# Optimization experiments

Hardware: AMD Instinct MI355X
Metric: run time of the kernel (lower is better)

The kernel has to match this reference:

```python
import jax, jax.numpy as jnp
import numpy as np

D = 512      # d_model
H = 8        # num_heads
DH = D // H  # d_head = 64
WIN = 10     # window_size
DFF = 2048   # d_ff
EPS = 1e-5   # LayerNorm eps


def _layernorm(x, w, b):
    mu = jnp.mean(x, axis=-1, keepdims=True)
    var = jnp.mean(jnp.square(x - mu), axis=-1, keepdims=True)
    return (x - mu) * jax.lax.rsqrt(var + EPS) * w + b


def setup_inputs() -> dict:
    key = jax.random.key(0)
    ks = jax.random.split(key, 8)
    s = 0.02
    inp = {
        "z": jax.random.normal(ks[0], (4, 2048, D), jnp.float32),
        "Wq": jax.random.normal(ks[1], (D, D), jnp.float32) * s,
        "bq": jnp.zeros((D,), jnp.float32),
        "Wk": jax.random.normal(ks[2], (D, D), jnp.float32) * s,
        "bk": jnp.zeros((D,), jnp.float32),
        "Wv": jax.random.normal(ks[3], (D, D), jnp.float32) * s,
        "bv": jnp.zeros((D,), jnp.float32),
        "Wo": jax.random.normal(ks[4], (D, D), jnp.float32) * s,
        "bo": jnp.zeros((D,), jnp.float32),
        "ln1_w": jnp.ones((D,), jnp.float32),
        "ln1_b": jnp.zeros((D,), jnp.float32),
        "W1": jax.random.normal(ks[5], (D, DFF), jnp.float32) * s,
        "b1": jnp.zeros((DFF,), jnp.float32),
        "W2": jax.random.normal(ks[6], (DFF, D), jnp.float32) * s,
        "b2": jnp.zeros((D,), jnp.float32),
        "ln2_w": jnp.ones((D,), jnp.float32),
        "ln2_b": jnp.zeros((D,), jnp.float32),
    }
    return inp


def reference(z, Wq, bq, Wk, bk, Wv, bv, Wo, bo, ln1_w, ln1_b, W1, b1, W2, b2, ln2_w, ln2_b):
    B, T, Dm = z.shape
    # projections -> [B, H, T, DH]
    q = (z @ Wq + bq).reshape(B, T, H, DH).transpose(0, 2, 1, 3)
    k = (z @ Wk + bk).reshape(B, T, H, DH).transpose(0, 2, 1, 3)
    v = (z @ Wv + bv).reshape(B, T, H, DH).transpose(0, 2, 1, 3)
    scale = 1.0 / jnp.sqrt(jnp.asarray(DH, z.dtype))
    scores = jnp.einsum('bhqd,bhkd->bhqk', q, k) * scale  # [B,H,T,T]
    idx = jnp.arange(T)
    dist = idx[:, None] - idx[None, :]
    valid = (dist >= 0) & (dist < WIN)
    neg = jnp.finfo(scores.dtype).min
    scores = jnp.where(valid[None, None], scores, neg)
    attn = jax.nn.softmax(scores, axis=-1)  # dropout is identity in eval
    out = jnp.einsum('bhqk,bhkd->bhqd', attn, v)
    out = out.transpose(0, 2, 1, 3).reshape(B, T, Dm)
    out = out @ Wo + bo
    z = _layernorm(z + out, ln1_w, ln1_b)
    # FFN with exact (erf) GELU, matching torch nn.GELU default
    ff = jax.nn.gelu(z @ W1 + b1, approximate=False) @ W2 + b2
    z = _layernorm(z + ff, ln2_w, ln2_b)
    return z
```

## Files before the change

### kernel.cpp

```cpp
#include <hip/hip_runtime.h>
#include <cstdint>
#include <cstddef>

#define DEV __device__ __forceinline__

typedef __bf16 bf16x8 __attribute__((ext_vector_type(8)));
typedef float f32x4 __attribute__((ext_vector_type(4)));
typedef unsigned short us8 __attribute__((ext_vector_type(8)));
typedef unsigned short us4 __attribute__((ext_vector_type(4)));

typedef const __attribute__((address_space(1))) unsigned int GUI;
typedef __attribute__((address_space(3))) unsigned int LUI;

DEV unsigned short f2bf(float f) {
  unsigned int u = __builtin_bit_cast(unsigned int, f);
  u += 0x7fffu + ((u >> 16) & 1u);
  return (unsigned short)(u >> 16);
}
DEV float bf2f(unsigned short h) {
  unsigned int u = ((unsigned int)h) << 16;
  return __builtin_bit_cast(float, u);
}

DEV void tr32(const float* __restrict__ in, unsigned short* __restrict__ out,
              int K, int N, int k0, int n0) {
  __shared__ float tile[32][33];
  const int tx = threadIdx.x & 31, ty = threadIdx.x >> 5;
#pragma unroll
  for (int i = 0; i < 32; i += 8)
    tile[ty + i][tx] = in[(size_t)(k0 + ty + i) * N + n0 + tx];
  __syncthreads();
#pragma unroll
  for (int i = 0; i < 32; i += 8)
    out[(size_t)(n0 + ty + i) * K + k0 + tx] = f2bf(tile[tx][ty + i]);
}

__global__ __launch_bounds__(256) void k_prep(
    const float* __restrict__ z, unsigned short* __restrict__ zb,
    const float* __restrict__ Wq, const float* __restrict__ Wk,
    const float* __restrict__ Wv, const float* __restrict__ Wo,
    unsigned short* __restrict__ Wsq,
    const float* __restrict__ W1, unsigned short* __restrict__ W1T,
    const float* __restrict__ W2, unsigned short* __restrict__ W2T,
    const float* __restrict__ bq, const float* __restrict__ bk,
    const float* __restrict__ bv, float* __restrict__ biasqkv) {
  const int j = blockIdx.x;
  const int tid = threadIdx.x;
  if (j < 4096) {
    int i = j * 256 + tid;
    float4 v = ((const float4*)z)[i];
    us4 o;
    o.x = f2bf(v.x); o.y = f2bf(v.y); o.z = f2bf(v.z); o.w = f2bf(v.w);
    *(us4*)(zb + (size_t)i * 4) = o;
  } else if (j < 5120) {
    int t = j - 4096;
    int mat = t >> 8, tile = t & 255;
    const float* in = mat == 0 ? Wq : mat == 1 ? Wk : mat == 2 ? Wv : Wo;
    tr32(in, Wsq + (size_t)mat * 262144, 512, 512, (tile >> 4) * 32, (tile & 15) * 32);
  } else if (j < 6144) {
    int t = j - 5120;
    tr32(W1, W1T, 512, 2048, (t / 64) * 32, (t % 64) * 32);
  } else if (j < 7168) {
    int t = j - 6144;
    tr32(W2, W2T, 2048, 512, (t / 16) * 32, (t % 16) * 32);
  } else {
    for (int i = tid; i < 1536; i += 256)
      biasqkv[i] = (i < 512) ? bq[i] : (i < 1024 ? bk[i - 512] : bv[i - 1024]);
  }
}

template <int MODE, int SPLITK>
DEV void gemm_body(const unsigned short* __restrict__ A,
                   const unsigned short* __restrict__ BT,
                   const float* __restrict__ bias,
                   unsigned short* __restrict__ outp,
                   int K, int N) {
  __shared__ __align__(16) unsigned short As[2 * 16384];
  __shared__ __align__(16) unsigned short Bs[2 * 16384];
  const int tid = threadIdx.x;
  const int wave = tid >> 6, lane = tid & 63;
  const int wm = wave >> 2, wn = wave & 3;
  const int q = lane >> 4, l15 = lane & 15;

  const int nx = gridDim.x, ny = gridDim.y;
  const int nwg = nx * ny * SPLITK;
  const int lid = (blockIdx.z * ny + blockIdx.y) * nx + blockIdx.x;
  const int q8 = nwg >> 3, r8 = nwg & 7;
  const int xcd = lid & 7, slot = lid >> 3;
  const int wid = (xcd < r8 ? xcd * (q8 + 1) : r8 * (q8 + 1) + (xcd - r8) * q8) + slot;
  const int nbz = nx * SPLITK;
  const int bxz = wid % nbz;
  const int by  = wid / nbz;
  const int bx  = bxz % nx;
  const int z   = bxz / nx;

  const int rbase = by * 256;
  const int nbase = bx * 256;
  const int nkt = (K / SPLITK) >> 6;
  const int kb = z * (K / SPLITK);

  float bv_[4];
#pragma unroll
  for (int n = 0; n < 4; ++n) {
    int gcol = nbase + wn * 64 + n * 16 + l15;
    bv_[n] = (z == 0) ? bias[gcol] : 0.f;
  }
  asm volatile("s_waitcnt vmcnt(0)" ::: "memory");

  auto STAGE2 = [&](int buf, int k0, int t0) {
#pragma unroll
    for (int t = t0; t < t0 + 2; ++t) {
      int s = t * 512 + tid;
      int row = s >> 3;
      int col = ((s & 7) ^ (row & 7)) << 3;
      const unsigned short* ga = A + (size_t)(rbase + row) * K + k0 + col;
      const unsigned short* gb = BT + (size_t)(nbase + row) * K + k0 + col;
      const int dst = buf * 16384 + (t * 512 + wave * 64) * 8;
      __builtin_amdgcn_global_load_lds((GUI*)ga, (LUI*)(As + dst), 16, 0, 0);
      __builtin_amdgcn_global_load_lds((GUI*)gb, (LUI*)(Bs + dst), 16, 0, 0);
    }
  };

  auto LDA = [&](const unsigned short* Ab, int ks, int mh, bf16x8* af) {
#pragma unroll
    for (int m = 0; m < 4; ++m) {
      int row = wm * 128 + (mh * 4 + m) * 16 + l15;
      int ch = (ks * 4 + q) ^ (row & 7);
      af[m] = __builtin_bit_cast(bf16x8, *(const us8*)(Ab + row * 64 + ch * 8));
    }
  };
  auto LDB = [&](const unsigned short* Bb, int ks, bf16x8* bfr) {
#pragma unroll
    for (int n = 0; n < 4; ++n) {
      int row = wn * 64 + n * 16 + l15;
      int ch = (ks * 4 + q) ^ (row & 7);
      bfr[n] = __builtin_bit_cast(bf16x8, *(const us8*)(Bb + row * 64 + ch * 8));
    }
  };

  f32x4 acc[8][4] = {};
  bf16x8 af[4], bfr0[4], bfr1[4];

  STAGE2(0, kb, 0);
  STAGE2(0, kb, 2);
  asm volatile("s_waitcnt vmcnt(0)" ::: "memory");
  __builtin_amdgcn_s_barrier();

#define PHASE_TAIL                                     \
  asm volatile("s_waitcnt lgkmcnt(0)" ::: "memory");   \
  __builtin_amdgcn_sched_barrier(0);                   \
  __builtin_amdgcn_s_setprio(1);

#define MFMA16(AF, BF, MH)                                                        \
  _Pragma("unroll") for (int m = 0; m < 4; ++m)                                   \
  _Pragma("unroll") for (int n = 0; n < 4; ++n)                                   \
    acc[MH * 4 + m][n] = __builtin_amdgcn_mfma_f32_16x16x32_bf16(AF[m], BF[n], acc[MH * 4 + m][n], 0, 0, 0);

  for (int t = 0; t < nkt; ++t) {
    const int cur = t & 1;
    const unsigned short* Ab = As + cur * 16384;
    const unsigned short* Bb = Bs + cur * 16384;
    const bool pre = (t + 1 < nkt);
    const int knext = kb + (t + 1) * 64;

    LDA(Ab, 0, 0, af);
    LDB(Bb, 0, bfr0);
    if (pre) STAGE2(cur ^ 1, knext, 0);
    __builtin_amdgcn_s_barrier();
    PHASE_TAIL
    MFMA16(af, bfr0, 0)
    __builtin_amdgcn_s_setprio(0);
    __builtin_amdgcn_s_barrier();

    LDA(Ab, 1, 0, af);
    LDB(Bb, 1, bfr1);
    if (pre) STAGE2(cur ^ 1, knext, 2);
    __builtin_amdgcn_s_barrier();
    PHASE_TAIL
    MFMA16(af, bfr1, 0)
    __builtin_amdgcn_s_setprio(0);
    __builtin_amdgcn_s_barrier();

    LDA(Ab, 0, 1, af);
    __builtin_amdgcn_s_barrier();
    PHASE_TAIL
    MFMA16(af, bfr0, 1)
    __builtin_amdgcn_s_setprio(0);
    __builtin_amdgcn_s_barrier();

    LDA(Ab, 1, 1, af);
    if (pre) asm volatile("s_waitcnt vmcnt(0)" ::: "memory");
    __builtin_amdgcn_s_barrier();
    PHASE_TAIL
    MFMA16(af, bfr1, 1)
    __builtin_amdgcn_s_setprio(0);
    __builtin_amdgcn_s_barrier();
  }
#undef PHASE_TAIL
#undef MFMA16

  unsigned short* opv = outp + (size_t)z * 8192 * N;
#pragma unroll
  for (int m = 0; m < 8; ++m) {
    int grow0 = rbase + wm * 128 + m * 16 + (q << 2);
#pragma unroll
    for (int n = 0; n < 4; ++n) {
      int gcol = nbase + wn * 64 + n * 16 + l15;
#pragma unroll
      for (int r = 0; r < 4; ++r) {
        float v = acc[m][n][r] + bv_[n];
        if (MODE == 2) v = 0.5f * v * (1.0f + erff(v * 0.70710678118654752f));
        opv[(size_t)(grow0 + r) * N + gcol] = f2bf(v);
      }
    }
  }
}

__global__ __launch_bounds__(512) void k_qkv(const unsigned short* __restrict__ A,
                                             const unsigned short* __restrict__ BT,
                                             const float* __restrict__ bias,
                                             unsigned short* __restrict__ outp, int K, int N) {
  gemm_body<0, 1>(A, BT, bias, outp, K, N);
}
__global__ __launch_bounds__(512) void k_wo(const unsigned short* __restrict__ A,
                                            const unsigned short* __restrict__ BT,
                                            const float* __restrict__ bias,
                                            unsigned short* __restrict__ outp, int K, int N) {
  gemm_body<0, 4>(A, BT, bias, outp, K, N);
}
__global__ __launch_bounds__(512) void k_ffn1(const unsigned short* __restrict__ A,
                                              const unsigned short* __restrict__ BT,
                                              const float* __restrict__ bias,
                                              unsigned short* __restrict__ outp, int K, int N) {
  gemm_body<2, 1>(A, BT, bias, outp, K, N);
}
__global__ __launch_bounds__(512) void k_ffn2(const unsigned short* __restrict__ A,
                                              const unsigned short* __restrict__ BT,
                                              const float* __restrict__ bias,
                                              unsigned short* __restrict__ outp, int K, int N) {
  gemm_body<0, 4>(A, BT, bias, outp, K, N);
}

__global__ __launch_bounds__(64) void k_attn(const unsigned short* __restrict__ qkv,
                                             unsigned short* __restrict__ attnb) {
  __shared__ float Qt[64 * 35];
  __shared__ float Kt[64 * 45];
  __shared__ float P[32 * 12];

  const int lane = threadIdx.x;
  const int bid = blockIdx.x;
  const int chunk = bid & 63;
  const int bh = bid >> 6;
  const int h = bh & 7, b = bh >> 3;
  const int i0 = chunk * 32;
  const int b2048 = b * 2048;
  const int h64 = h * 64;

#pragma unroll 8
  for (int r = 0; r < 41; ++r) {
    int jloc = i0 - 9 + r;
    int jc = jloc < 0 ? 0 : jloc;
    Kt[lane * 45 + r] = bf2f(qkv[(size_t)(b2048 + jc) * 1536 + 512 + h64 + lane]);
  }
#pragma unroll 8
  for (int r = 0; r < 32; ++r) {
    Qt[lane * 35 + r] = bf2f(qkv[(size_t)(b2048 + i0 + r) * 1536 + h64 + lane]);
  }
  __syncthreads();

  const int qe = lane & 31, dh = lane >> 5;
  float s[10];
#pragma unroll
  for (int jj = 0; jj < 10; ++jj) s[jj] = 0.f;
#pragma unroll
  for (int dd = 0; dd < 32; ++dd) {
    int d = dh * 32 + dd;
    float qd = Qt[d * 35 + qe];
#pragma unroll
    for (int jj = 0; jj < 10; ++jj)
      s[jj] = fmaf(qd, Kt[d * 45 + qe + jj], s[jj]);
  }
#pragma unroll
  for (int jj = 0; jj < 10; ++jj) s[jj] += __shfl_xor(s[jj], 32);

  const int iG = i0 + qe;
#pragma unroll
  for (int jj = 0; jj < 10; ++jj)
    s[jj] = (iG - 9 + jj >= 0) ? s[jj] * 0.125f : -1e30f;
  float mx = s[9];
#pragma unroll
  for (int jj = 0; jj < 9; ++jj) mx = fmaxf(mx, s[jj]);
  float den = 0.f;
#pragma unroll
  for (int jj = 0; jj < 10; ++jj) {
    s[jj] = __expf(s[jj] - mx);
    den += s[jj];
  }
  float inv = 1.f / den;
  if (lane < 32) {
#pragma unroll
    for (int jj = 0; jj < 10; ++jj) P[qe * 12 + jj] = s[jj] * inv;
  }
  __syncthreads();

  for (int q0 = 0; q0 < 32; q0 += 4) {
    float vv[13];
#pragma unroll
    for (int t = 0; t < 13; ++t) {
      int jloc = i0 + q0 - 9 + t;
      int jc = jloc < 0 ? 0 : jloc;
      vv[t] = bf2f(qkv[(size_t)(b2048 + jc) * 1536 + 1024 + h64 + lane]);
    }
#pragma unroll
    for (int qq = 0; qq < 4; ++qq) {
      const int qy = q0 + qq;
      const float* pp = &P[qy * 12];
      float o = 0.f;
#pragma unroll
      for (int jj = 0; jj < 10; ++jj) o = fmaf(pp[jj], vv[qq + jj], o);
      attnb[(size_t)(b2048 + i0 + qy) * 512 + h64 + lane] = f2bf(o);
    }
  }
}

template <int OUTF32, int NP>
DEV void ln_body(const unsigned short* __restrict__ res,
                 const unsigned short* __restrict__ add,
                 const float* __restrict__ w,
                 const float* __restrict__ bb,
                 void* __restrict__ outp) {
  const size_t PLANE = (size_t)8192 * 512;
  const int wave = threadIdx.x >> 6, lane = threadIdx.x & 63;
  const int row = blockIdx.x * 4 + wave;
  float x[8];
  us8 r = *(const us8*)(res + (size_t)row * 512 + lane * 8);
#pragma unroll
  for (int j = 0; j < 8; ++j) x[j] = bf2f(r[j]);
#pragma unroll
  for (int p = 0; p < NP; ++p) {
    us8 a = *(const us8*)(add + p * PLANE + (size_t)row * 512 + lane * 8);
#pragma unroll
    for (int j = 0; j < 8; ++j) x[j] += bf2f(a[j]);
  }
  float sum = 0.f, ss = 0.f;
#pragma unroll
  for (int j = 0; j < 8; ++j) {
    sum += x[j];
    ss += x[j] * x[j];
  }
#pragma unroll
  for (int m = 32; m >= 1; m >>= 1) {
    sum += __shfl_xor(sum, m);
    ss += __shfl_xor(ss, m);
  }
  const float mu = sum * (1.f / 512.f);
  float var = ss * (1.f / 512.f) - mu * mu;
  const float rstd = rsqrtf(var + 1e-5f);
  const int c = lane * 8;
  float o[8];
#pragma unroll
  for (int j = 0; j < 8; ++j) o[j] = (x[j] - mu) * rstd * w[c + j] + bb[c + j];
  if (OUTF32 == 0) {
    us8 u;
#pragma unroll
    for (int j = 0; j < 8; ++j) u[j] = f2bf(o[j]);
    *(us8*)((unsigned short*)outp + (size_t)row * 512 + c) = u;
  } else {
    float4 u0, u1;
    u0.x = o[0]; u0.y = o[1]; u0.z = o[2]; u0.w = o[3];
    u1.x = o[4]; u1.y = o[5]; u1.z = o[6]; u1.w = o[7];
    float4* o4 = (float4*)((float*)outp + (size_t)row * 512 + c);
    o4[0] = u0; o4[1] = u1;
  }
}

__global__ __launch_bounds__(256) void k_ln_mid(const unsigned short* __restrict__ res,
                                                const unsigned short* __restrict__ add,
                                                const float* __restrict__ w,
                                                const float* __restrict__ bb,
                                                unsigned short* __restrict__ outp) {
  ln_body<0, 4>(res, add, w, bb, outp);
}
__global__ __launch_bounds__(256) void k_ln_out(const unsigned short* __restrict__ res,
                                                const unsigned short* __restrict__ add,
                                                const float* __restrict__ w,
                                                const float* __restrict__ bb,
                                                float* __restrict__ outp) {
  ln_body<1, 4>(res, add, w, bb, outp);
}

extern "C" void kernel_launch(void* const* d_in, const int* in_sizes, int n_in,
                              void* d_out, int out_size, void* d_ws, size_t ws_size,
                              hipStream_t stream) {
  const float* z    = (const float*)d_in[0];
  const float* Wq   = (const float*)d_in[1];
  const float* bq   = (const float*)d_in[2];
  const float* Wk   = (const float*)d_in[3];
  const float* bk   = (const float*)d_in[4];
  const float* Wv   = (const float*)d_in[5];
  const float* bv   = (const float*)d_in[6];
  const float* Wo   = (const float*)d_in[7];
  const float* bo   = (const float*)d_in[8];
  const float* ln1w = (const float*)d_in[9];
  const float* ln1b = (const float*)d_in[10];
  const float* W1   = (const float*)d_in[11];
  const float* b1   = (const float*)d_in[12];
  const float* W2   = (const float*)d_in[13];
  const float* b2   = (const float*)d_in[14];
  const float* ln2w = (const float*)d_in[15];
  const float* ln2b = (const float*)d_in[16];
  float* out = (float*)d_out;

  char* ws = (char*)d_ws;
  size_t off = 0;
  auto alloc = [&](size_t bytes) {
    char* p = ws + off;
    off += (bytes + 255) & ~(size_t)255;
    return p;
  };
  unsigned short* Wsq   = (unsigned short*)alloc((size_t)2048 * 512 * 2);
  unsigned short* WTqkv = Wsq;
  unsigned short* WoT   = Wsq + (size_t)1536 * 512;
  unsigned short* W1T   = (unsigned short*)alloc((size_t)2048 * 512 * 2);
  unsigned short* W2T   = (unsigned short*)alloc((size_t)512 * 2048 * 2);
  float*          biasqkv = (float*)alloc(1536 * 4);
  unsigned short* zb    = (unsigned short*)alloc((size_t)8192 * 512 * 2);
  unsigned short* z1b   = (unsigned short*)alloc((size_t)8192 * 512 * 2);
  unsigned short* qkvb  = (unsigned short*)alloc((size_t)8192 * 1536 * 2);
  unsigned short* attnb = (unsigned short*)alloc((size_t)8192 * 512 * 2);
  unsigned short* p1    = (unsigned short*)alloc((size_t)4 * 8192 * 512 * 2);
  unsigned short* ff    = qkvb;

  k_prep<<<7169, 256, 0, stream>>>(z, zb, Wq, Wk, Wv, Wo, Wsq, W1, W1T, W2, W2T,
                                   bq, bk, bv, biasqkv);
  k_qkv<<<dim3(6, 32), 512, 0, stream>>>(zb, WTqkv, biasqkv, qkvb, 512, 1536);
  k_attn<<<2048, 64, 0, stream>>>(qkvb, attnb);
  k_wo<<<dim3(2, 32, 4), 512, 0, stream>>>(attnb, WoT, bo, p1, 512, 512);
  k_ln_mid<<<2048, 256, 0, stream>>>(zb, p1, ln1w, ln1b, z1b);
  k_ffn1<<<dim3(8, 32), 512, 0, stream>>>(z1b, W1T, b1, ff, 512, 2048);
  k_ffn2<<<dim3(2, 32, 4), 512, 0, stream>>>(ff, W2T, b2, p1, 2048, 512);
  k_ln_out<<<2048, 256, 0, stream>>>(z1b, p1, ln2w, ln2b, out);
}
```

Before: 145.0 us.

## Switch GEMM to four-stage K=32 LDS pipeline with precomputed addresses

Restructures the GEMM main loop from a double-buffered K=64 tile to a four-slot ring buffer of K=32 tiles, prefetching three tiles ahead and waiting with partial vmcnt counts instead of full drains. It changes the LDS layout so two rows share a 64-element line, and precomputes the global and LDS fragment offsets once outside the loop. The goal is to hide global-load latency better and cut per-iteration address arithmetic. In exchange there are twice as many iterations with barriers, and the hand-tuned vmcnt counts must exactly match the number of loads still in flight.

Measured after the change: 147.1 us. Within noise of the previous version (+1.4%).

```diff
diff --git a/kernel.cpp b/kernel.cpp
--- a/kernel.cpp
+++ b/kernel.cpp
@@ -75,8 +75,8 @@
                    const float* __restrict__ bias,
                    unsigned short* __restrict__ outp,
                    int K, int N) {
-  __shared__ __align__(16) unsigned short As[2 * 16384];
-  __shared__ __align__(16) unsigned short Bs[2 * 16384];
+  __shared__ __align__(16) unsigned short As[4 * 8192];
+  __shared__ __align__(16) unsigned short Bs[4 * 8192];
   const int tid = threadIdx.x;
   const int wave = tid >> 6, lane = tid & 63;
   const int wm = wave >> 2, wn = wave & 3;
@@ -86,8 +86,8 @@
   const int nwg = nx * ny * SPLITK;
   const int lid = (blockIdx.z * ny + blockIdx.y) * nx + blockIdx.x;
   const int q8 = nwg >> 3, r8 = nwg & 7;
-  const int xcd = lid & 7, slot = lid >> 3;
-  const int wid = (xcd < r8 ? xcd * (q8 + 1) : r8 * (q8 + 1) + (xcd - r8) * q8) + slot;
+  const int xcd = lid & 7, slot0 = lid >> 3;
+  const int wid = (xcd < r8 ? xcd * (q8 + 1) : r8 * (q8 + 1) + (xcd - r8) * q8) + slot0;
   const int nbz = nx * SPLITK;
   const int bxz = wid % nbz;
   const int by  = wid / nbz;
@@ -96,7 +96,7 @@
 
   const int rbase = by * 256;
   const int nbase = bx * 256;
-  const int nkt = (K / SPLITK) >> 6;
+  const int nkt = (K / SPLITK) >> 5;
   const int kb = z * (K / SPLITK);
 
   float bv_[4];
@@ -107,97 +107,107 @@
   }
   asm volatile("s_waitcnt vmcnt(0)" ::: "memory");
 
-  auto STAGE2 = [&](int buf, int k0, int t0) {
-#pragma unroll
-    for (int t = t0; t < t0 + 2; ++t) {
-      int s = t * 512 + tid;
-      int row = s >> 3;
-      int col = ((s & 7) ^ (row & 7)) << 3;
-      const unsigned short* ga = A + (size_t)(rbase + row) * K + k0 + col;
-      const unsigned short* gb = BT + (size_t)(nbase + row) * K + k0 + col;
-      const int dst = buf * 16384 + (t * 512 + wave * 64) * 8;
-      __builtin_amdgcn_global_load_lds((GUI*)ga, (LUI*)(As + dst), 16, 0, 0);
-      __builtin_amdgcn_global_load_lds((GUI*)gb, (LUI*)(Bs + dst), 16, 0, 0);
-    }
-  };
-
-  auto LDA = [&](const unsigned short* Ab, int ks, int mh, bf16x8* af) {
-#pragma unroll
-    for (int m = 0; m < 4; ++m) {
-      int row = wm * 128 + (mh * 4 + m) * 16 + l15;
-      int ch = (ks * 4 + q) ^ (row & 7);
-      af[m] = __builtin_bit_cast(bf16x8, *(const us8*)(Ab + row * 64 + ch * 8));
-    }
-  };
-  auto LDB = [&](const unsigned short* Bb, int ks, bf16x8* bfr) {
-#pragma unroll
-    for (int n = 0; n < 4; ++n) {
-      int row = wn * 64 + n * 16 + l15;
-      int ch = (ks * 4 + q) ^ (row & 7);
-      bfr[n] = __builtin_bit_cast(bf16x8, *(const us8*)(Bb + row * 64 + ch * 8));
-    }
-  };
+  const unsigned short* pA[2];
+  const unsigned short* pB[2];
+  int dstL[2];
+#pragma unroll
+  for (int i = 0; i < 2; ++i) {
+    int s = i * 512 + tid;
+    int R = s >> 3;
+    int c = (s & 7) ^ (R & 7);
+    int r = 2 * R + (c >> 2);
+    int kl = (c & 3) << 3;
+    pA[i] = A + (size_t)(rbase + r) * K + kb + kl;
+    pB[i] = BT + (size_t)(nbase + r) * K + kb + kl;
+    dstL[i] = (i * 512 + wave * 64) * 8;
+  }
+  const unsigned short* pA0 = pA[0]; const unsigned short* pA1 = pA[1];
+  const unsigned short* pB0 = pB[0]; const unsigned short* pB1 = pB[1];
+
+#define STAGE_A(SLOT)                                                                     \
+  __builtin_amdgcn_global_load_lds((GUI*)pA0, (LUI*)(As + (SLOT) * 8192 + dstL[0]), 16, 0, 0); \
+  __builtin_amdgcn_global_load_lds((GUI*)pA1, (LUI*)(As + (SLOT) * 8192 + dstL[1]), 16, 0, 0); \
+  pA0 += 32; pA1 += 32;
+#define STAGE_B(SLOT)                                                                     \
+  __builtin_amdgcn_global_load_lds((GUI*)pB0, (LUI*)(Bs + (SLOT) * 8192 + dstL[0]), 16, 0, 0); \
+  __builtin_amdgcn_global_load_lds((GUI*)pB1, (LUI*)(Bs + (SLOT) * 8192 + dstL[1]), 16, 0, 0); \
+  pB0 += 32; pB1 += 32;
+
+  int aoff[8], boff[4];
+#pragma unroll
+  for (int m = 0; m < 8; ++m) {
+    int rr = wm * 128 + m * 16 + l15;
+    int R = rr >> 1;
+    int d = (((rr & 1) << 2) + q) ^ (R & 7);
+    aoff[m] = R * 64 + d * 8;
+  }
+#pragma unroll
+  for (int n = 0; n < 4; ++n) {
+    int rr = wn * 64 + n * 16 + l15;
+    int R = rr >> 1;
+    int d = (((rr & 1) << 2) + q) ^ (R & 7);
+    boff[n] = R * 64 + d * 8;
+  }
 
   f32x4 acc[8][4] = {};
-  bf16x8 af[4], bfr0[4], bfr1[4];
-
-  STAGE2(0, kb, 0);
-  STAGE2(0, kb, 2);
-  asm volatile("s_waitcnt vmcnt(0)" ::: "memory");
+  bf16x8 af[4], bfr[4];
+
+  STAGE_A(0) STAGE_B(0)
+  STAGE_A(1) STAGE_B(1)
+  STAGE_A(2) STAGE_B(2)
+  asm volatile("s_waitcnt vmcnt(8)" ::: "memory");
   __builtin_amdgcn_s_barrier();
 
-#define PHASE_TAIL                                     \
-  asm volatile("s_waitcnt lgkmcnt(0)" ::: "memory");   \
-  __builtin_amdgcn_sched_barrier(0);                   \
-  __builtin_amdgcn_s_setprio(1);
-
-#define MFMA16(AF, BF, MH)                                                        \
-  _Pragma("unroll") for (int m = 0; m < 4; ++m)                                   \
-  _Pragma("unroll") for (int n = 0; n < 4; ++n)                                   \
-    acc[MH * 4 + m][n] = __builtin_amdgcn_mfma_f32_16x16x32_bf16(AF[m], BF[n], acc[MH * 4 + m][n], 0, 0, 0);
+#define MFMA16(MH)                                                                 \
+  _Pragma("unroll") for (int m = 0; m < 4; ++m)                                    \
+  _Pragma("unroll") for (int n = 0; n < 4; ++n)                                    \
+    acc[(MH) * 4 + m][n] =                                                         \
+        __builtin_amdgcn_mfma_f32_16x16x32_bf16(af[m], bfr[n], acc[(MH) * 4 + m][n], 0, 0, 0);
 
   for (int t = 0; t < nkt; ++t) {
-    const int cur = t & 1;
-    const unsigned short* Ab = As + cur * 16384;
-    const unsigned short* Bb = Bs + cur * 16384;
-    const bool pre = (t + 1 < nkt);
-    const int knext = kb + (t + 1) * 64;
-
-    LDA(Ab, 0, 0, af);
-    LDB(Bb, 0, bfr0);
-    if (pre) STAGE2(cur ^ 1, knext, 0);
+    const int slot = t & 3;
+    const unsigned short* Ab = As + slot * 8192;
+    const unsigned short* Bb = Bs + slot * 8192;
+    const bool pre = (t + 3 < nkt);
+    const int nslot = (t + 3) & 3;
+
+#pragma unroll
+    for (int m = 0; m < 4; ++m)
+      af[m] = __builtin_bit_cast(bf16x8, *(const us8*)(Ab + aoff[m]));
+#pragma unroll
+    for (int n = 0; n < 4; ++n)
+      bfr[n] = __builtin_bit_cast(bf16x8, *(const us8*)(Bb + boff[n]));
+    if (pre) { STAGE_A(nslot) }
     __builtin_amdgcn_s_barrier();
-    PHASE_TAIL
-    MFMA16(af, bfr0, 0)
+    asm volatile("s_waitcnt lgkmcnt(0)" ::: "memory");
+    __builtin_amdgcn_sched_barrier(0);
+    __builtin_amdgcn_s_setprio(1);
+    MFMA16(0)
     __builtin_amdgcn_s_setprio(0);
     __builtin_amdgcn_s_barrier();
 
-    LDA(Ab, 1, 0, af);
-    LDB(Bb, 1, bfr1);
-    if (pre) STAGE2(cur ^ 1, knext, 2);
+#pragma unroll
+    for (int m = 0; m < 4; ++m)
+      af[m] = __builtin_bit_cast(bf16x8, *(const us8*)(Ab + aoff[4 + m]));
+    if (pre) {
+      STAGE_B(nslot)
+      asm volatile("s_waitcnt vmcnt(8)" ::: "memory");
+    } else if (t + 2 < nkt) {
+      asm volatile("s_waitcnt vmcnt(4)" ::: "memory");
+    } else if (t + 1 < nkt) {
+      asm volatile("s_waitcnt vmcnt(0)" ::: "memory");
+    }
     __builtin_amdgcn_s_barrier();
-    PHASE_TAIL
-    MFMA16(af, bfr1, 0)
+    asm volatile("s_waitcnt lgkmcnt(0)" ::: "memory");
+    __builtin_amdgcn_sched_barrier(0);
+    __builtin_amdgcn_s_setprio(1);
+    MFMA16(1)
     __builtin_amdgcn_s_setprio(0);
     __builtin_amdgcn_s_barrier();
-
-    LDA(Ab, 0, 1, af);
-    __builtin_amdgcn_s_barrier();
-    PHASE_TAIL
-    MFMA16(af, bfr0, 1)
-    __builtin_amdgcn_s_setprio(0);
-    __builtin_amdgcn_s_barrier();
-
-    LDA(Ab, 1, 1, af);
-    if (pre) asm volatile("s_waitcnt vmcnt(0)" ::: "memory");
-    __builtin_amdgcn_s_barrier();
-    PHASE_TAIL
-    MFMA16(af, bfr1, 1)
-    __builtin_amdgcn_s_setprio(0);
-    __builtin_amdgcn_s_barrier();
-  }
-#undef PHASE_TAIL
+  }
 #undef MFMA16
+#undef STAGE_A
+#undef STAGE_B
 
   unsigned short* opv = outp + (size_t)z * 8192 * N;
 #pragma unroll
```

## Switch GEMMs to 128x128 tiles, drop split-K, simplify pipeline

Applied to the files above, without the earlier changes.

Replaces the 256x256 tile GEMM with 8 waves and a 4-phase interleaved schedule by a 128x128 tile GEMM with 4 waves and a simple double-buffered loop. Split-K is removed from the Wo and FFN2 GEMMs, so the layernorm kernels now read a single partial instead of summing four planes. This launches more, smaller workgroups and cuts partial-sum traffic and LDS use per block. The cost is less operand reuse per tile and a less finely tuned overlap between loads and MFMA work.

After: 147.7 us. Within noise of the previous version (+1.8%).

```diff
diff --git a/kernel.cpp b/kernel.cpp
--- a/kernel.cpp
+++ b/kernel.cpp
@@ -69,140 +69,94 @@
   }
 }
 
-template <int MODE, int SPLITK>
+template <int MODE>
 DEV void gemm_body(const unsigned short* __restrict__ A,
                    const unsigned short* __restrict__ BT,
                    const float* __restrict__ bias,
                    unsigned short* __restrict__ outp,
                    int K, int N) {
-  __shared__ __align__(16) unsigned short As[2 * 16384];
-  __shared__ __align__(16) unsigned short Bs[2 * 16384];
+  __shared__ __align__(16) unsigned short As[2 * 8192];
+  __shared__ __align__(16) unsigned short Bs[2 * 8192];
   const int tid = threadIdx.x;
   const int wave = tid >> 6, lane = tid & 63;
-  const int wm = wave >> 2, wn = wave & 3;
+  const int wm = wave >> 1, wn = wave & 1;
   const int q = lane >> 4, l15 = lane & 15;
 
   const int nx = gridDim.x, ny = gridDim.y;
-  const int nwg = nx * ny * SPLITK;
-  const int lid = (blockIdx.z * ny + blockIdx.y) * nx + blockIdx.x;
+  const int nwg = nx * ny;
+  const int lid = blockIdx.y * nx + blockIdx.x;
   const int q8 = nwg >> 3, r8 = nwg & 7;
   const int xcd = lid & 7, slot = lid >> 3;
   const int wid = (xcd < r8 ? xcd * (q8 + 1) : r8 * (q8 + 1) + (xcd - r8) * q8) + slot;
-  const int nbz = nx * SPLITK;
-  const int bxz = wid % nbz;
-  const int by  = wid / nbz;
-  const int bx  = bxz % nx;
-  const int z   = bxz / nx;
-
-  const int rbase = by * 256;
-  const int nbase = bx * 256;
-  const int nkt = (K / SPLITK) >> 6;
-  const int kb = z * (K / SPLITK);
+  const int bx = wid % nx;
+  const int by = wid / nx;
+
+  const int rbase = by * 128;
+  const int nbase = bx * 128;
+  const int nkt = K >> 6;
 
   float bv_[4];
 #pragma unroll
-  for (int n = 0; n < 4; ++n) {
-    int gcol = nbase + wn * 64 + n * 16 + l15;
-    bv_[n] = (z == 0) ? bias[gcol] : 0.f;
-  }
+  for (int n = 0; n < 4; ++n) bv_[n] = bias[nbase + wn * 64 + n * 16 + l15];
   asm volatile("s_waitcnt vmcnt(0)" ::: "memory");
 
-  auto STAGE2 = [&](int buf, int k0, int t0) {
-#pragma unroll
-    for (int t = t0; t < t0 + 2; ++t) {
-      int s = t * 512 + tid;
+  auto STAGE = [&](int buf, int k0) {
+#pragma unroll
+    for (int t = 0; t < 4; ++t) {
+      int s = t * 256 + tid;
       int row = s >> 3;
       int col = ((s & 7) ^ (row & 7)) << 3;
       const unsigned short* ga = A + (size_t)(rbase + row) * K + k0 + col;
       const unsigned short* gb = BT + (size_t)(nbase + row) * K + k0 + col;
-      const int dst = buf * 16384 + (t * 512 + wave * 64) * 8;
+      const int dst = buf * 8192 + (t * 256 + wave * 64) * 8;
       __builtin_amdgcn_global_load_lds((GUI*)ga, (LUI*)(As + dst), 16, 0, 0);
       __builtin_amdgcn_global_load_lds((GUI*)gb, (LUI*)(Bs + dst), 16, 0, 0);
     }
   };
 
-  auto LDA = [&](const unsigned short* Ab, int ks, int mh, bf16x8* af) {
-#pragma unroll
-    for (int m = 0; m < 4; ++m) {
-      int row = wm * 128 + (mh * 4 + m) * 16 + l15;
-      int ch = (ks * 4 + q) ^ (row & 7);
-      af[m] = __builtin_bit_cast(bf16x8, *(const us8*)(Ab + row * 64 + ch * 8));
-    }
-  };
-  auto LDB = [&](const unsigned short* Bb, int ks, bf16x8* bfr) {
-#pragma unroll
-    for (int n = 0; n < 4; ++n) {
-      int row = wn * 64 + n * 16 + l15;
-      int ch = (ks * 4 + q) ^ (row & 7);
-      bfr[n] = __builtin_bit_cast(bf16x8, *(const us8*)(Bb + row * 64 + ch * 8));
-    }
-  };
-
-  f32x4 acc[8][4] = {};
-  bf16x8 af[4], bfr0[4], bfr1[4];
-
-  STAGE2(0, kb, 0);
-  STAGE2(0, kb, 2);
-  asm volatile("s_waitcnt vmcnt(0)" ::: "memory");
-  __builtin_amdgcn_s_barrier();
-
-#define PHASE_TAIL                                     \
-  asm volatile("s_waitcnt lgkmcnt(0)" ::: "memory");   \
-  __builtin_amdgcn_sched_barrier(0);                   \
-  __builtin_amdgcn_s_setprio(1);
-
-#define MFMA16(AF, BF, MH)                                                        \
-  _Pragma("unroll") for (int m = 0; m < 4; ++m)                                   \
-  _Pragma("unroll") for (int n = 0; n < 4; ++n)                                   \
-    acc[MH * 4 + m][n] = __builtin_amdgcn_mfma_f32_16x16x32_bf16(AF[m], BF[n], acc[MH * 4 + m][n], 0, 0, 0);
-
-  for (int t = 0; t < nkt; ++t) {
-    const int cur = t & 1;
-    const unsigned short* Ab = As + cur * 16384;
-    const unsigned short* Bb = Bs + cur * 16384;
-    const bool pre = (t + 1 < nkt);
-    const int knext = kb + (t + 1) * 64;
-
-    LDA(Ab, 0, 0, af);
-    LDB(Bb, 0, bfr0);
-    if (pre) STAGE2(cur ^ 1, knext, 0);
+  f32x4 acc[4][4] = {};
+  STAGE(0, 0);
+
+  for (int kt = 0; kt < nkt; ++kt) {
+    const int cur = kt & 1;
+    if (kt + 1 < nkt) {
+      STAGE(cur ^ 1, (kt + 1) * 64);
+      asm volatile("s_waitcnt vmcnt(8)" ::: "memory");
+    } else {
+      asm volatile("s_waitcnt vmcnt(0)" ::: "memory");
+    }
     __builtin_amdgcn_s_barrier();
-    PHASE_TAIL
-    MFMA16(af, bfr0, 0)
-    __builtin_amdgcn_s_setprio(0);
+
+#pragma unroll
+    for (int ks = 0; ks < 2; ++ks) {
+      bf16x8 af[4], bfr[4];
+#pragma unroll
+      for (int m = 0; m < 4; ++m) {
+        int row = wm * 64 + m * 16 + l15;
+        int ch = (ks * 4 + q) ^ (row & 7);
+        af[m] = __builtin_bit_cast(bf16x8, *(const us8*)(As + cur * 8192 + row * 64 + ch * 8));
+      }
+#pragma unroll
+      for (int n = 0; n < 4; ++n) {
+        int row = wn * 64 + n * 16 + l15;
+        int ch = (ks * 4 + q) ^ (row & 7);
+        bfr[n] = __builtin_bit_cast(bf16x8, *(const us8*)(Bs + cur * 8192 + row * 64 + ch * 8));
+      }
+      __builtin_amdgcn_s_setprio(1);
+#pragma unroll
+      for (int m = 0; m < 4; ++m)
+#pragma unroll
+        for (int n = 0; n < 4; ++n)
+          acc[m][n] = __builtin_amdgcn_mfma_f32_16x16x32_bf16(af[m], bfr[n], acc[m][n], 0, 0, 0);
+      __builtin_amdgcn_s_setprio(0);
+    }
+    asm volatile("s_waitcnt lgkmcnt(0)" ::: "memory");
     __builtin_amdgcn_s_barrier();
-
-    LDA(Ab, 1, 0, af);
-    LDB(Bb, 1, bfr1);
-    if (pre) STAGE2(cur ^ 1, knext, 2);
-    __builtin_amdgcn_s_barrier();
-    PHASE_TAIL
-    MFMA16(af, bfr1, 0)
-    __builtin_amdgcn_s_setprio(0);
-    __builtin_amdgcn_s_barrier();
-
-    LDA(Ab, 0, 1, af);
-    __builtin_amdgcn_s_barrier();
-    PHASE_TAIL
-    MFMA16(af, bfr0, 1)
-    __builtin_amdgcn_s_setprio(0);
-    __builtin_amdgcn_s_barrier();
-
-    LDA(Ab, 1, 1, af);
-    if (pre) asm volatile("s_waitcnt vmcnt(0)" ::: "memory");
-    __builtin_amdgcn_s_barrier();
-    PHASE_TAIL
-    MFMA16(af, bfr1, 1)
-    __builtin_amdgcn_s_setprio(0);
-    __builtin_amdgcn_s_barrier();
-  }
-#undef PHASE_TAIL
-#undef MFMA16
-
-  unsigned short* opv = outp + (size_t)z * 8192 * N;
-#pragma unroll
-  for (int m = 0; m < 8; ++m) {
-    int grow0 = rbase + wm * 128 + m * 16 + (q << 2);
+  }
+
+#pragma unroll
+  for (int m = 0; m < 4; ++m) {
+    int grow0 = rbase + wm * 64 + m * 16 + (q << 2);
 #pragma unroll
     for (int n = 0; n < 4; ++n) {
       int gcol = nbase + wn * 64 + n * 16 + l15;
@@ -210,35 +164,35 @@
       for (int r = 0; r < 4; ++r) {
         float v = acc[m][n][r] + bv_[n];
         if (MODE == 2) v = 0.5f * v * (1.0f + erff(v * 0.70710678118654752f));
-        opv[(size_t)(grow0 + r) * N + gcol] = f2bf(v);
+        outp[(size_t)(grow0 + r) * N + gcol] = f2bf(v);
       }
     }
   }
 }
 
-__global__ __launch_bounds__(512) void k_qkv(const unsigned short* __restrict__ A,
+__global__ __launch_bounds__(256) void k_qkv(const unsigned short* __restrict__ A,
                                              const unsigned short* __restrict__ BT,
                                              const float* __restrict__ bias,
                                              unsigned short* __restrict__ outp, int K, int N) {
-  gemm_body<0, 1>(A, BT, bias, outp, K, N);
-}
-__global__ __launch_bounds__(512) void k_wo(const unsigned short* __restrict__ A,
+  gemm_body<0>(A, BT, bias, outp, K, N);
+}
+__global__ __launch_bounds__(256) void k_wo(const unsigned short* __restrict__ A,
                                             const unsigned short* __restrict__ BT,
                                             const float* __restrict__ bias,
                                             unsigned short* __restrict__ outp, int K, int N) {
-  gemm_body<0, 4>(A, BT, bias, outp, K, N);
-}
-__global__ __launch_bounds__(512) void k_ffn1(const unsigned short* __restrict__ A,
+  gemm_body<0>(A, BT, bias, outp, K, N);
+}
+__global__ __launch_bounds__(256) void k_ffn1(const unsigned short* __restrict__ A,
                                               const unsigned short* __restrict__ BT,
                                               const float* __restrict__ bias,
                                               unsigned short* __restrict__ outp, int K, int N) {
-  gemm_body<2, 1>(A, BT, bias, outp, K, N);
-}
-__global__ __launch_bounds__(512) void k_ffn2(const unsigned short* __restrict__ A,
+  gemm_body<2>(A, BT, bias, outp, K, N);
+}
+__global__ __launch_bounds__(256) void k_ffn2(const unsigned short* __restrict__ A,
                                               const unsigned short* __restrict__ BT,
                                               const float* __restrict__ bias,
                                               unsigned short* __restrict__ outp, int K, int N) {
-  gemm_body<0, 4>(A, BT, bias, outp, K, N);
+  gemm_body<0>(A, BT, bias, outp, K, N);
 }
 
 __global__ __launch_bounds__(64) void k_attn(const unsigned short* __restrict__ qkv,
@@ -323,28 +277,21 @@
   }
 }
 
-template <int OUTF32, int NP>
+template <int OUTF32>
 DEV void ln_body(const unsigned short* __restrict__ res,
                  const unsigned short* __restrict__ add,
                  const float* __restrict__ w,
                  const float* __restrict__ bb,
                  void* __restrict__ outp) {
-  const size_t PLANE = (size_t)8192 * 512;
   const int wave = threadIdx.x >> 6, lane = threadIdx.x & 63;
   const int row = blockIdx.x * 4 + wave;
   float x[8];
   us8 r = *(const us8*)(res + (size_t)row * 512 + lane * 8);
-#pragma unroll
-  for (int j = 0; j < 8; ++j) x[j] = bf2f(r[j]);
-#pragma unroll
-  for (int p = 0; p < NP; ++p) {
-    us8 a = *(const us8*)(add + p * PLANE + (size_t)row * 512 + lane * 8);
-#pragma unroll
-    for (int j = 0; j < 8; ++j) x[j] += bf2f(a[j]);
-  }
+  us8 a = *(const us8*)(add + (size_t)row * 512 + lane * 8);
   float sum = 0.f, ss = 0.f;
 #pragma unroll
   for (int j = 0; j < 8; ++j) {
+    x[j] = bf2f(r[j]) + bf2f(a[j]);
     sum += x[j];
     ss += x[j] * x[j];
   }
@@ -379,14 +326,14 @@
                                                 const float* __restrict__ w,
                                                 const float* __restrict__ bb,
                                                 unsigned short* __restrict__ outp) {
-  ln_body<0, 4>(res, add, w, bb, outp);
+  ln_body<0>(res, add, w, bb, outp);
 }
 __global__ __launch_bounds__(256) void k_ln_out(const unsigned short* __restrict__ res,
                                                 const unsigned short* __restrict__ add,
                                                 const float* __restrict__ w,
                                                 const float* __restrict__ bb,
                                                 float* __restrict__ outp) {
-  ln_body<1, 4>(res, add, w, bb, outp);
+  ln_body<1>(res, add, w, bb, outp);
 }
 
 extern "C" void kernel_launch(void* const* d_in, const int* in_sizes, int n_in,
@@ -428,16 +375,17 @@
   unsigned short* z1b   = (unsigned short*)alloc((size_t)8192 * 512 * 2);
   unsigned short* qkvb  = (unsigned short*)alloc((size_t)8192 * 1536 * 2);
   unsigned short* attnb = (unsigned short*)alloc((size_t)8192 * 512 * 2);
-  unsigned short* p1    = (unsigned short*)alloc((size_t)4 * 8192 * 512 * 2);
+  unsigned short* woout = (unsigned short*)alloc((size_t)8192 * 512 * 2);
+  unsigned short* f2out = (unsigned short*)alloc((size_t)8192 * 512 * 2);
   unsigned short* ff    = qkvb;
 
   k_prep<<<7169, 256, 0, stream>>>(z, zb, Wq, Wk, Wv, Wo, Wsq, W1, W1T, W2, W2T,
                                    bq, bk, bv, biasqkv);
-  k_qkv<<<dim3(6, 32), 512, 0, stream>>>(zb, WTqkv, biasqkv, qkvb, 512, 1536);
+  k_qkv<<<dim3(12, 64), 256, 0, stream>>>(zb, WTqkv, biasqkv, qkvb, 512, 1536);
   k_attn<<<2048, 64, 0, stream>>>(qkvb, attnb);
-  k_wo<<<dim3(2, 32, 4), 512, 0, stream>>>(attnb, WoT, bo, p1, 512, 512);
-  k_ln_mid<<<2048, 256, 0, stream>>>(zb, p1, ln1w, ln1b, z1b);
-  k_ffn1<<<dim3(8, 32), 512, 0, stream>>>(z1b, W1T, b1, ff, 512, 2048);
-  k_ffn2<<<dim3(2, 32, 4), 512, 0, stream>>>(ff, W2T, b2, p1, 2048, 512);
-  k_ln_out<<<2048, 256, 0, stream>>>(z1b, p1, ln2w, ln2b, out);
-}
+  k_wo<<<dim3(4, 64), 256, 0, stream>>>(attnb, WoT, bo, woout, 512, 512);
+  k_ln_mid<<<2048, 256, 0, stream>>>(zb, woout, ln1w, ln1b, z1b);
+  k_ffn1<<<dim3(16, 64), 256, 0, stream>>>(z1b, W1T, b1, ff, 512, 2048);
+  k_ffn2<<<dim3(4, 64), 256, 0, stream>>>(ff, W2T, b2, f2out, 2048, 512);
+  k_ln_out<<<2048, 256, 0, stream>>>(z1b, f2out, ln2w, ln2b, out);
+}
```
